# Performance work log

Hardware: AMD Instinct MI355X
Metric: run time of the kernel (lower is better)

The kernel has to match this reference:

```python
import jax, jax.numpy as jnp
import numpy as np

B, S, D, H, L = 8, 4096, 512, 512, 2


def log_g(x):
    # log of g(x) where g(x) = x + 0.5 for x >= 0 else sigmoid(x)
    return jnp.where(x >= 0, jnp.log(jax.nn.relu(x) + 0.5), -jax.nn.softplus(-x))


def g(x):
    return jnp.where(x >= 0, x + 0.5, jax.nn.sigmoid(x))


def mingru_layer(x, h0, wz, bz, wh, bh):
    """Log-space parallel-scan minGRU layer.
    x: (B,S,Din), h0: (B,1,H) positive (already g-activated).
    wz,wh: (H,Din); bz,bh: (H,). Returns full hidden sequence (B,S,H)."""
    k = jnp.einsum('bsd,hd->bsh', x, wz) + bz          # gate pre-activation
    log_z = -jax.nn.softplus(-k)                        # log sigmoid(k)
    log_coeffs = -jax.nn.softplus(k)                    # log(1 - sigmoid(k))
    log_h_tilde = log_g(jnp.einsum('bsd,hd->bsh', x, wh) + bh)
    log_values = log_z + log_h_tilde                    # log(z * h_tilde)
    log_h0 = jnp.log(h0)                                # (B,1,H)
    # Heinsen associative scan in log space
    a_star = jnp.cumsum(
        jnp.concatenate([jnp.zeros_like(log_h0), log_coeffs], axis=1), axis=1)  # (B,S+1,H)
    log_vals = jnp.concatenate([log_h0, log_values], axis=1)                     # (B,S+1,H)
    log_h = a_star + jax.lax.cumlogsumexp(log_vals - a_star, axis=1)
    return jnp.exp(log_h)[:, 1:]                        # (B,S,H)


def setup_inputs() -> dict:
    key = jax.random.key(0)
    ks = jax.random.split(key, 1 + 4 * L)
    x = jax.random.normal(ks[0], (B, S, D), dtype=jnp.float32)
    inp = {'x': x}
    dims_in = [D] + [H] * (L - 1)
    i = 1
    for l in range(L):
        din = dims_in[l]
        stdv = 1.0 / np.sqrt(din)
        inp[f'wz{l}'] = jax.random.uniform(ks[i], (H, din), minval=-stdv, maxval=stdv); i += 1
        inp[f'bz{l}'] = jax.random.uniform(ks[i], (H,), minval=-stdv, maxval=stdv); i += 1
        inp[f'wh{l}'] = jax.random.uniform(ks[i], (H, din), minval=-stdv, maxval=stdv); i += 1
        inp[f'bh{l}'] = jax.random.uniform(ks[i], (H,), minval=-stdv, maxval=stdv); i += 1
    return inp


def reference(x, wz0, bz0, wh0, bh0, wz1, bz1, wh1, bh1):
    # h is None -> h0 = g(zeros) = 0.5 for every layer
    h0 = jnp.full((B, 1, H), 0.5, dtype=x.dtype)
    params = [(wz0, bz0, wh0, bh0), (wz1, bz1, wh1, bh1)]
    inp = x
    finals = []
    for (wz, bz, wh, bh) in params:
        out = mingru_layer(inp, h0, wz, bz, wh, bh)
        finals.append(out[:, -1:])
        inp = out  # Identity layer transform, no residual, dropout=0
    return out, jnp.stack(finals)  # (B,S,H), (L,B,1,H)
```

## Files before the change

kernel.cpp:

```cpp
#include <hip/hip_runtime.h>
#include <math.h>

#define BB 8
#define SS 4096
#define DD 512
#define HH 512
#define MM (BB*SS)

constexpr int TCH = 64;
constexpr int NC  = SS / TCH;
constexpr int BH  = BB * HH;

constexpr int BM = 128;
constexpr int BN = 64;
constexpr int BK = 64;

typedef short  short8  __attribute__((ext_vector_type(8)));
typedef float  float4v __attribute__((ext_vector_type(4)));

__device__ inline unsigned short f2bf(float f) {
    union { float f; unsigned u; } v; v.f = f;
    unsigned r = v.u + 0x7FFF + ((v.u >> 16) & 1);
    return (unsigned short)(r >> 16);
}
__device__ inline float bf_lo(unsigned u) {
    union { unsigned u; float f; } x; x.u = u << 16; return x.f;
}
__device__ inline float bf_hi(unsigned u) {
    union { unsigned u; float f; } x; x.u = u & 0xffff0000u; return x.f;
}
__device__ inline float fast_rcp(float x) {
    return __builtin_amdgcn_rcpf(x);
}

__device__ inline void async_copy16(const void* g, void* l) {
    __builtin_amdgcn_global_load_lds(
        (const __attribute__((address_space(1))) void*)g,
        (__attribute__((address_space(3))) void*)l, 16, 0, 0);
}

__global__ __launch_bounds__(256)
void conv_all(const float* __restrict__ x,
              const float* __restrict__ w0, const float* __restrict__ w1,
              const float* __restrict__ w2, const float* __restrict__ w3,
              short* __restrict__ Xbf, short* __restrict__ Wbf)
{
    constexpr int XBLK = MM * DD / 8 / 256;
    constexpr int WBLK = HH * DD / 8 / 256;
    const int bid = blockIdx.x;
    const float* src; short* dst; size_t base;
    if (bid < XBLK) {
        src = x; dst = Xbf;
        base = ((size_t)bid * 256 + threadIdx.x) * 8;
    } else {
        const int idx  = bid - XBLK;
        const int wsel = idx / WBLK;
        src = (wsel == 0) ? w0 : (wsel == 1) ? w1 : (wsel == 2) ? w2 : w3;
        dst = Wbf + (size_t)wsel * HH * DD;
        base = ((size_t)(idx % WBLK) * 256 + threadIdx.x) * 8;
    }
    float4 a = *(const float4*)(src + base);
    float4 b = *(const float4*)(src + base + 4);
    short8 r;
    r[0] = f2bf(a.x); r[1] = f2bf(a.y); r[2] = f2bf(a.z); r[3] = f2bf(a.w);
    r[4] = f2bf(b.x); r[5] = f2bf(b.y); r[6] = f2bf(b.z); r[7] = f2bf(b.w);
    *(short8*)(dst + base) = r;
}

__global__ __launch_bounds__(256)
void gemm_gate_mfma(const short* __restrict__ Xg, const short* __restrict__ Wz,
                    const float* __restrict__ bz, const short* __restrict__ Wh,
                    const float* __restrict__ bh, unsigned* __restrict__ AV,
                    float2* __restrict__ cAV)
{
    __shared__ char smem[32768];
    short*    lds    = (short*)smem;
    unsigned* lds_av = (unsigned*)smem;
    constexpr int ZOFF = BM * BK;
    constexpr int HOFF = BM * BK + BN * BK;

    const int t    = threadIdx.x;
    const int wave = t >> 6;
    const int lane = t & 63;
    const int col16 = lane & 15;
    const int quad  = lane >> 4;
    const int wm = wave >> 1;
    const int wn = wave & 1;
    const int m0 = blockIdx.x * BM;
    const int n0 = blockIdx.y * BN;

    float4v accz[4][2], acch[4][2];
    #pragma unroll
    for (int i = 0; i < 4; ++i)
        #pragma unroll
        for (int j = 0; j < 2; ++j) {
            accz[i][j] = (float4v){0.f, 0.f, 0.f, 0.f};
            acch[i][j] = (float4v){0.f, 0.f, 0.f, 0.f};
        }

    const int lr = lane >> 3;
    const int lc = (lane & 7) * 8;

    for (int k0 = 0; k0 < DD; k0 += BK) {
        #pragma unroll
        for (int i = 0; i < 4; ++i) {
            const int r0 = wave * 32 + i * 8;
            async_copy16(Xg + (size_t)(m0 + r0 + lr) * DD + k0 + lc,
                         &lds[r0 * BK]);
        }
        #pragma unroll
        for (int i = 0; i < 2; ++i) {
            const int r0 = wave * 16 + i * 8;
            async_copy16(Wz + (size_t)(n0 + r0 + lr) * DD + k0 + lc,
                         &lds[ZOFF + r0 * BK]);
            async_copy16(Wh + (size_t)(n0 + r0 + lr) * DD + k0 + lc,
                         &lds[HOFF + r0 * BK]);
        }
        __syncthreads();

        #pragma unroll
        for (int kk = 0; kk < 2; ++kk) {
            short8 af[4], bzf[2], bhf[2];
            #pragma unroll
            for (int mi = 0; mi < 4; ++mi)
                af[mi] = *(const short8*)&lds[(wm*64 + mi*16 + col16) * BK + kk*32 + quad*8];
            #pragma unroll
            for (int nj = 0; nj < 2; ++nj) {
                bzf[nj] = *(const short8*)&lds[ZOFF + (wn*32 + nj*16 + col16) * BK + kk*32 + quad*8];
                bhf[nj] = *(const short8*)&lds[HOFF + (wn*32 + nj*16 + col16) * BK + kk*32 + quad*8];
            }
            #pragma unroll
            for (int mi = 0; mi < 4; ++mi)
                #pragma unroll
                for (int nj = 0; nj < 2; ++nj) {
                    accz[mi][nj] = __builtin_amdgcn_mfma_f32_16x16x32_bf16(af[mi], bzf[nj], accz[mi][nj], 0, 0, 0);
                    acch[mi][nj] = __builtin_amdgcn_mfma_f32_16x16x32_bf16(af[mi], bhf[nj], acch[mi][nj], 0, 0, 0);
                }
        }
        __syncthreads();
    }

    #pragma unroll
    for (int nj = 0; nj < 2; ++nj) {
        const int ln = wn*32 + nj*16 + col16;
        const int n  = n0 + ln;
        const float bzn = bz[n], bhn = bh[n];
        #pragma unroll
        for (int mi = 0; mi < 4; ++mi) {
            const int lmb = wm*64 + mi*16 + quad*4;
            #pragma unroll
            for (int reg = 0; reg < 4; ++reg) {
                const float kz = accz[mi][nj][reg] + bzn;
                const float kh = acch[mi][nj][reg] + bhn;
                const float a  = fast_rcp(1.0f + __expf(kz));
                const float sn = fast_rcp(1.0f + __expf(-kh));
                const float ht = (kh >= 0.0f) ? (kh + 0.5f) : sn;
                const float v  = (1.0f - a) * ht;
                lds_av[(lmb + reg) * 64 + ln] = ((unsigned)f2bf(v) << 16) | f2bf(a);
            }
        }
    }
    __syncthreads();

    {
        const int row0 = t >> 4;
        const int col  = (t & 15) * 4;
        #pragma unroll
        for (int i = 0; i < 8; ++i) {
            const int row = row0 + i * 16;
            const uint4 u = *(const uint4*)&lds_av[row * 64 + col];
            *(uint4*)&AV[(size_t)(m0 + row) * HH + n0 + col] = u;
        }
    }

    {
        const int task = t >> 1;
        const int hf   = t & 1;
        const int c    = task >> 6;
        const int ln   = task & 63;
        float prod = 1.0f, hl = 0.0f;
        #pragma unroll 8
        for (int s = 0; s < TCH / 2; ++s) {
            const unsigned u = lds_av[(c * TCH + hf * 32 + s) * 64 + ln];
            const float a = bf_lo(u), v = bf_hi(u);
            hl   = fmaf(a, hl, v);
            prod *= a;
        }
        const float pA = __shfl_xor(prod, 1);
        const float pV = __shfl_xor(hl, 1);
        if (hf == 0) {
            const int b  = m0 >> 12;
            const int cg = ((m0 & 4095) >> 6) + c;
            cAV[(size_t)cg * BH + b * HH + (n0 + ln)] =
                make_float2(prod * pA, fmaf(pA, hl, pV));
        }
    }
}

__global__ __launch_bounds__(256)
void scan_apply_f32(const unsigned* __restrict__ AV,
                    const float2* __restrict__ cAV,
                    float* __restrict__ out, float* __restrict__ finals)
{
    const int h = blockIdx.x * 256 + threadIdx.x;
    const int b = blockIdx.y;
    const int c = blockIdx.z;
    const int ch = b * HH + h;
    float hcur = 0.5f;
    for (int cp = 0; cp < c; ++cp) {
        const float2 s = cAV[(size_t)cp * BH + ch];
        hcur = fmaf(s.x, hcur, s.y);
    }
    size_t base = ((size_t)(b * SS + c * TCH)) * HH + h;
    #pragma unroll 8
    for (int tt = 0; tt < TCH; ++tt) {
        const unsigned u = AV[base];
        hcur = fmaf(bf_lo(u), hcur, bf_hi(u));
        out[base] = hcur;
        base += HH;
    }
    if (c == NC - 1) finals[ch] = hcur;
}

__global__ __launch_bounds__(256)
void scan_apply_bf16(const unsigned* __restrict__ AV,
                     const float2* __restrict__ cAV,
                     short* __restrict__ out, float* __restrict__ finals)
{
    const int h = blockIdx.x * 256 + threadIdx.x;
    const int b = blockIdx.y;
    const int c = blockIdx.z;
    const int ch = b * HH + h;
    float hcur = 0.5f;
    for (int cp = 0; cp < c; ++cp) {
        const float2 s = cAV[(size_t)cp * BH + ch];
        hcur = fmaf(s.x, hcur, s.y);
    }
    size_t base = ((size_t)(b * SS + c * TCH)) * HH + h;
    #pragma unroll 8
    for (int tt = 0; tt < TCH; ++tt) {
        const unsigned u = AV[base];
        hcur = fmaf(bf_lo(u), hcur, bf_hi(u));
        out[base] = (short)f2bf(hcur);
        base += HH;
    }
    if (c == NC - 1) finals[ch] = hcur;
}

extern "C" void kernel_launch(void* const* d_in, const int* in_sizes, int n_in,
                              void* d_out, int out_size, void* d_ws, size_t ws_size,
                              hipStream_t stream)
{
    const float* x   = (const float*)d_in[0];
    const float* wz0 = (const float*)d_in[1];
    const float* bz0 = (const float*)d_in[2];
    const float* wh0 = (const float*)d_in[3];
    const float* bh0 = (const float*)d_in[4];
    const float* wz1 = (const float*)d_in[5];
    const float* bz1 = (const float*)d_in[6];
    const float* wh1 = (const float*)d_in[7];
    const float* bh1 = (const float*)d_in[8];

    float* out    = (float*)d_out;
    float* finals = out + (size_t)MM * HH;

    unsigned* AV  = (unsigned*)d_ws;
    short* Xbf    = (short*)(AV + (size_t)MM * HH);
    short* Wbf    = Xbf + (size_t)MM * DD;
    float2* cAV   = (float2*)(Wbf + (size_t)4 * HH * DD);

    short* Wz0 = Wbf;
    short* Wh0 = Wbf + (size_t)1 * HH * DD;
    short* Wz1 = Wbf + (size_t)2 * HH * DD;
    short* Wh1 = Wbf + (size_t)3 * HH * DD;

    const dim3 gg(MM / BM, HH / BN);
    const dim3 gs(HH / 256, BB, NC);

    conv_all<<<MM * DD / 8 / 256 + 4 * (HH * DD / 8 / 256), 256, 0, stream>>>(
        x, wz0, wh0, wz1, wh1, Xbf, Wbf);

    gemm_gate_mfma <<<gg, 256, 0, stream>>>(Xbf, Wz0, bz0, Wh0, bh0, AV, cAV);
    scan_apply_bf16<<<gs, 256, 0, stream>>>(AV, cAV, Xbf, finals);

    gemm_gate_mfma <<<gg, 256, 0, stream>>>(Xbf, Wz1, bz1, Wh1, bh1, AV, cAV);
    scan_apply_f32 <<<gs, 256, 0, stream>>>(AV, cAV, out, finals + BH);
}
```

Before: 312.9 us.

## Double-buffer gate GEMM LDS tiles and XOR-swizzle to avoid bank conflicts

The gate GEMM now keeps two LDS buffers and issues the async copies for the next K-slice before computing on the current one, so global loads overlap MFMA work. Per-iteration syncthreads become explicit vmcnt/lgkmcnt waits plus an s_barrier. Global source columns are XOR-permuted by row, and the fragment reads use a matching XOR offset, to spread LDS bank accesses. LDS use doubles to 64KB, which can reduce how many blocks fit per CU.

```diff
diff --git a/kernel.cpp b/kernel.cpp
--- a/kernel.cpp
+++ b/kernel.cpp
@@ -73,11 +73,13 @@
                     const float* __restrict__ bh, unsigned* __restrict__ AV,
                     float2* __restrict__ cAV)
 {
-    __shared__ char smem[32768];
+    __shared__ char smem[65536];
     short*    lds    = (short*)smem;
     unsigned* lds_av = (unsigned*)smem;
+    constexpr int BUFS = 16384;
     constexpr int ZOFF = BM * BK;
-    constexpr int HOFF = BM * BK + BN * BK;
+    constexpr int HOFF = ZOFF + BN * BK;
+    constexpr int NIT  = DD / BK;
 
     const int t    = threadIdx.x;
     const int wave = t >> 6;
@@ -98,36 +100,50 @@
             acch[i][j] = (float4v){0.f, 0.f, 0.f, 0.f};
         }
 
-    const int lr = lane >> 3;
-    const int lc = (lane & 7) * 8;
-
-    for (int k0 = 0; k0 < DD; k0 += BK) {
+    const int lr  = lane >> 3;
+    const int lcs = (((lane & 7) ^ lr) * 8);
+
+    auto stage = [&](int buf, int k0) {
+        short* L = lds + buf * BUFS;
         #pragma unroll
         for (int i = 0; i < 4; ++i) {
             const int r0 = wave * 32 + i * 8;
-            async_copy16(Xg + (size_t)(m0 + r0 + lr) * DD + k0 + lc,
-                         &lds[r0 * BK]);
+            async_copy16(Xg + (size_t)(m0 + r0 + lr) * DD + k0 + lcs,
+                         &L[r0 * BK]);
         }
         #pragma unroll
         for (int i = 0; i < 2; ++i) {
             const int r0 = wave * 16 + i * 8;
-            async_copy16(Wz + (size_t)(n0 + r0 + lr) * DD + k0 + lc,
-                         &lds[ZOFF + r0 * BK]);
-            async_copy16(Wh + (size_t)(n0 + r0 + lr) * DD + k0 + lc,
-                         &lds[HOFF + r0 * BK]);
-        }
-        __syncthreads();
-
+            async_copy16(Wz + (size_t)(n0 + r0 + lr) * DD + k0 + lcs,
+                         &L[ZOFF + r0 * BK]);
+            async_copy16(Wh + (size_t)(n0 + r0 + lr) * DD + k0 + lcs,
+                         &L[HOFF + r0 * BK]);
+        }
+    };
+
+    stage(0, 0);
+    asm volatile("s_waitcnt vmcnt(0)" ::: "memory");
+    __builtin_amdgcn_s_barrier();
+    asm volatile("" ::: "memory");
+
+    const int swz = (col16 & 7) * 8;
+
+    #pragma unroll
+    for (int it = 0; it < NIT; ++it) {
+        if (it + 1 < NIT) stage((it + 1) & 1, (it + 1) * BK);
+
+        const short* L = lds + (it & 1) * BUFS;
         #pragma unroll
         for (int kk = 0; kk < 2; ++kk) {
+            const int ko = (kk * 32 + quad * 8) ^ swz;
             short8 af[4], bzf[2], bhf[2];
             #pragma unroll
             for (int mi = 0; mi < 4; ++mi)
-                af[mi] = *(const short8*)&lds[(wm*64 + mi*16 + col16) * BK + kk*32 + quad*8];
+                af[mi] = *(const short8*)&L[(wm*64 + mi*16 + col16) * BK + ko];
             #pragma unroll
             for (int nj = 0; nj < 2; ++nj) {
-                bzf[nj] = *(const short8*)&lds[ZOFF + (wn*32 + nj*16 + col16) * BK + kk*32 + quad*8];
-                bhf[nj] = *(const short8*)&lds[HOFF + (wn*32 + nj*16 + col16) * BK + kk*32 + quad*8];
+                bzf[nj] = *(const short8*)&L[ZOFF + (wn*32 + nj*16 + col16) * BK + ko];
+                bhf[nj] = *(const short8*)&L[HOFF + (wn*32 + nj*16 + col16) * BK + ko];
             }
             #pragma unroll
             for (int mi = 0; mi < 4; ++mi)
@@ -137,7 +153,9 @@
                     acch[mi][nj] = __builtin_amdgcn_mfma_f32_16x16x32_bf16(af[mi], bhf[nj], acch[mi][nj], 0, 0, 0);
                 }
         }
-        __syncthreads();
+        asm volatile("s_waitcnt vmcnt(0) lgkmcnt(0)" ::: "memory");
+        __builtin_amdgcn_s_barrier();
+        asm volatile("" ::: "memory");
     }
 
     #pragma unroll
```

Measured after the change: 295.7 us. 5.5% less time.
